# Kernel optimization log

Hardware: AMD Instinct MI355X
Metric: run time of the kernel (lower is better)

Reference implementation:

```python
import jax, jax.numpy as jnp
import numpy as np

N = 400_000
G = 160
C_IN, C_OUT = 64, 38
K = 27  # 3x3x3 kernel offsets


def _build_neighbor_map(rng):
    # sample N unique occupied voxel coordinates, sorted by ravelled key
    keys = np.sort(rng.choice(G ** 3, size=N, replace=False))
    coords = np.stack(np.unravel_index(keys, (G, G, G)), axis=1).astype(np.int64)  # [N,3]
    nbr = np.full((K, N), N, dtype=np.int32)  # N = padding index -> zero feature row
    k = 0
    for dx in (-1, 0, 1):
        for dy in (-1, 0, 1):
            for dz in (-1, 0, 1):
                nc = coords + np.array([dx, dy, dz])
                valid = np.all((nc >= 0) & (nc < G), axis=1)
                nkey = (nc[:, 0] * G + nc[:, 1]) * G + nc[:, 2]
                pos = np.searchsorted(keys, nkey)
                pos_c = np.clip(pos, 0, N - 1)
                found = valid & (keys[pos_c] == nkey)
                nbr[k] = np.where(found, pos_c, N).astype(np.int32)
                k += 1
    return nbr


def setup_inputs() -> dict:
    key = jax.random.key(0)
    k1, k2, k3 = jax.random.split(key, 3)
    rng = np.random.default_rng(0)
    neighbor_idx = jnp.asarray(_build_neighbor_map(rng))
    features = jax.random.normal(k1, (N, C_IN), dtype=jnp.float32)
    # kaiming_normal fan_out (relu): std = sqrt(2 / fan_out), fan_out = K * C_out
    std1 = (2.0 / (K * C_OUT)) ** 0.5
    std2 = (2.0 / (K * C_OUT)) ** 0.5
    W1 = jax.random.normal(k2, (K, C_IN, C_OUT), dtype=jnp.float32) * std1
    W2 = jax.random.normal(k3, (K, C_OUT, C_OUT), dtype=jnp.float32) * std2
    return {"features": features, "neighbor_idx": neighbor_idx, "W1": W1, "W2": W2}


def _sparse_conv(feat, W, neighbor_idx):
    # gather-GEMM-scatter: out[i] = sum_k W[k]^T feat[nbr[k,i]]
    fp = jnp.concatenate([feat, jnp.zeros((1, feat.shape[1]), feat.dtype)], axis=0)
    out = jnp.zeros((feat.shape[0], W.shape[2]), feat.dtype)
    for k in range(K):  # fixed structural loop over 27 kernel offsets
        out = out + fp[neighbor_idx[k]] @ W[k]
    return out


def reference(features, neighbor_idx, W1, W2):
    h = _sparse_conv(features, W1, neighbor_idx)
    h = jax.nn.gelu(h, approximate=False)  # torch nn.GELU default = exact
    return _sparse_conv(h, W2, neighbor_idx)
```

## Files before the change

kernel.cpp:

```cpp
#include <hip/hip_runtime.h>
#include <math.h>

#define NPTS 400000
#define K27  27
#define WSTRIDE 4096

typedef unsigned short u16;
typedef __bf16 bf16x8 __attribute__((ext_vector_type(8)));
typedef float  f32x4  __attribute__((ext_vector_type(4)));
typedef __attribute__((address_space(1))) void gvoid;
typedef __attribute__((address_space(3))) void lvoid;

__device__ __forceinline__ u16 f2bf(float f) {
    unsigned u = __float_as_uint(f);
    u += 0x7FFFu + ((u >> 16) & 1u);
    return (u16)(u >> 16);
}
__device__ __forceinline__ unsigned pack2(float lo, float hi) {
    return (unsigned)f2bf(lo) | ((unsigned)f2bf(hi) << 16);
}
__device__ __forceinline__ bf16x8 pack8(float4 x, float4 y) {
    union { uint4 u; bf16x8 v; } r;
    r.u.x = pack2(x.x, x.y); r.u.y = pack2(x.z, x.w);
    r.u.z = pack2(y.x, y.y); r.u.w = pack2(y.z, y.w);
    return r.v;
}
__device__ __forceinline__ bf16x8 zero8() {
    union { uint4 u; bf16x8 v; } r;
    r.u.x = 0; r.u.y = 0; r.u.z = 0; r.u.w = 0;
    return r.v;
}

__global__ void prep_w(const float* __restrict__ W1, const float* __restrict__ W2,
                       u16* __restrict__ W1t, u16* __restrict__ W2t,
                       u16* __restrict__ hpad, u16* __restrict__ fpad)
{
    int i = blockIdx.x * 256 + threadIdx.x;
    if (i < 64) {
        hpad[i] = 0;
        if (fpad) fpad[i] = 0;
    }
    const int TOT = K27 * 48 * 64;
    if (i >= TOT) return;
    int k  = i / (48 * 64);
    int r  = i % (48 * 64);
    int n  = r >> 6;
    int kc = r & 63;
    u16 w1 = 0, w2 = 0;
    if (n < 38) {
        w1 = f2bf(W1[(k * 64 + kc) * 38 + n]);
        if (kc < 38) w2 = f2bf(W2[(k * 38 + kc) * 38 + n]);
    }
    int os = r ^ ((n & 7) << 3);
    W1t[k * WSTRIDE + os] = w1;
    W2t[k * WSTRIDE + os] = w2;
}

__global__ void prep_feat(const float* __restrict__ F, u16* __restrict__ Fb)
{
    size_t i = (size_t)blockIdx.x * 256 + threadIdx.x;
    const size_t TOT = (size_t)NPTS * 64 / 8;
    if (i >= TOT) return;
    const float4* fp = (const float4*)(F + i * 8);
    float4 a = fp[0], b = fp[1];
    uint4 v;
    v.x = pack2(a.x, a.y); v.y = pack2(a.z, a.w);
    v.z = pack2(b.x, b.y); v.w = pack2(b.z, b.w);
    *(uint4*)(Fb + i * 8) = v;
}

template<int LAYER, bool BF16IN>
__global__ __launch_bounds__(256, 3)
void spconv(const void* __restrict__ in_, const int* __restrict__ nbr,
            const u16* __restrict__ Wt, void* __restrict__ out_)
{
    __shared__ __align__(16) u16 wbuf[2][WSTRIDE];

    const int t    = threadIdx.x;
    const int wave = t >> 6;
    const int lane = t & 63;
    const int quad = lane >> 4;
    const int l16  = lane & 15;

    int bid;
    {
        const int nwg = NPTS / 128, q = nwg / 8, r = nwg % 8;
        int x = blockIdx.x % 8, o = blockIdx.x / 8;
        bid = (x < r ? x * (q + 1) : r * (q + 1) + (x - r) * q) + o;
    }
    const int rbase = bid * 128 + wave * 32;
    const int swz   = (l16 & 7) << 3;

    f32x4 acc[2][3] = {};
    bf16x8 aP[2][2], aQ[2][2], aR[2][2];
    int jP[2], jQ[2], jR[2];

    #define GATHER_BF16(dst, ids)                                             \
        {                                                                     \
            const u16* F = (const u16*)in_;                                   \
            _Pragma("unroll")                                                 \
            for (int rt = 0; rt < 2; ++rt) {                                  \
                const u16* rowp = F + (size_t)(ids)[rt] * 64 + quad * 8;      \
                (dst)[rt][0] = *(const bf16x8*)(rowp);                        \
                (dst)[rt][1] = *(const bf16x8*)(rowp + 32);                   \
            }                                                                 \
        }
    #define GATHER_F32(dst, ids)                                              \
        {                                                                     \
            const float* F = (const float*)in_;                               \
            _Pragma("unroll")                                                 \
            for (int rt = 0; rt < 2; ++rt) {                                  \
                if ((ids)[rt] < NPTS) {                                       \
                    const float* rowp = F + (size_t)(ids)[rt] * 64 + quad * 8;\
                    float4 f0 = *(const float4*)(rowp);                       \
                    float4 f1 = *(const float4*)(rowp + 4);                   \
                    float4 f2 = *(const float4*)(rowp + 32);                  \
                    float4 f3 = *(const float4*)(rowp + 36);                  \
                    (dst)[rt][0] = pack8(f0, f1);                             \
                    (dst)[rt][1] = pack8(f2, f3);                             \
                } else {                                                      \
                    (dst)[rt][0] = zero8();                                   \
                    (dst)[rt][1] = zero8();                                   \
                }                                                             \
            }                                                                 \
        }
    #define GATHER(dst, ids) { if (BF16IN) GATHER_BF16(dst, ids) else GATHER_F32(dst, ids) }

    #define STAGE_W(KW, BSEL)                                                 \
        {                                                                     \
            const u16* g_ = Wt + (size_t)(KW) * WSTRIDE + t * 8;              \
            u16* l_ = &wbuf[(BSEL)][t * 8];                                   \
            __builtin_amdgcn_global_load_lds((gvoid*)(g_),                    \
                                             (lvoid*)(l_), 16, 0, 0);         \
            __builtin_amdgcn_global_load_lds((gvoid*)(g_ + 2048),             \
                                             (lvoid*)(l_ + 2048), 16, 0, 0);  \
        }

    {
        int i0[2], i1[2];
        #pragma unroll
        for (int rt = 0; rt < 2; ++rt) i0[rt] = nbr[rbase + rt * 16 + l16];
        GATHER(aP, i0);
        #pragma unroll
        for (int rt = 0; rt < 2; ++rt) i1[rt] = nbr[(size_t)NPTS + rbase + rt * 16 + l16];
        GATHER(aQ, i1);
        #pragma unroll
        for (int rt = 0; rt < 2; ++rt) jP[rt] = nbr[(size_t)2 * NPTS + rbase + rt * 16 + l16];
    }
    STAGE_W(0, 0);
    STAGE_W(1, 1);
    __builtin_amdgcn_sched_barrier(0);
    asm volatile("s_waitcnt vmcnt(2)");
    __builtin_amdgcn_s_barrier();
    __builtin_amdgcn_sched_barrier(0);

    #define ITER(KK, ACUR, AISS, JUSE, JLOAD)                                 \
      {                                                                       \
        const int k_ = (KK);                                                  \
        bf16x8 bfr[3][2];                                                     \
        {                                                                     \
            const u16* wb = &wbuf[k_ & 1][0];                                 \
            _Pragma("unroll")                                                 \
            for (int nt = 0; nt < 3; ++nt)                                    \
                _Pragma("unroll")                                             \
                for (int ks = 0; ks < 2; ++ks)                                \
                    bfr[nt][ks] = *(const bf16x8*)&wb[(nt * 16 + l16) * 64    \
                                        + ((ks * 32 + quad * 8) ^ swz)];      \
        }                                                                     \
        {                                                                     \
            int kf = k_ + 3; if (kf > K27 - 1) kf = K27 - 1;                  \
            const int* nr = nbr + (size_t)kf * NPTS + rbase;                  \
            _Pragma("unroll")                                                 \
            for (int rt = 0; rt < 2; ++rt) JLOAD[rt] = nr[rt * 16 + l16];     \
        }                                                                     \
        GATHER(AISS, JUSE);                                                   \
        __builtin_amdgcn_sched_barrier(0);                                    \
        __builtin_amdgcn_s_setprio(1);                                        \
        _Pragma("unroll")                                                     \
        for (int ks = 0; ks < 2; ++ks)                                        \
            _Pragma("unroll")                                                 \
            for (int rt = 0; rt < 2; ++rt)                                    \
                _Pragma("unroll")                                             \
                for (int nt = 0; nt < 3; ++nt)                                \
                    acc[rt][nt] = __builtin_amdgcn_mfma_f32_16x16x32_bf16(    \
                        ACUR[rt][ks], bfr[nt][ks], acc[rt][nt], 0, 0, 0);     \
        __builtin_amdgcn_s_setprio(0);                                        \
        __builtin_amdgcn_sched_barrier(0);                                    \
        if (BF16IN) { asm volatile("s_waitcnt vmcnt(6)"); }                   \
        else        { asm volatile("s_waitcnt vmcnt(10)"); }                  \
        __builtin_amdgcn_s_barrier();                                         \
        __builtin_amdgcn_sched_barrier(0);                                    \
        {                                                                     \
            int kw = k_ + 2; if (kw > K27 - 1) kw = K27 - 1;                  \
            STAGE_W(kw, k_ & 1);                                              \
        }                                                                     \
        __builtin_amdgcn_sched_barrier(0);                                    \
      }

    for (int k = 0; k < K27; k += 3) {
        ITER(k,     aP, aR, jP, jQ);
        ITER(k + 1, aQ, aP, jQ, jR);
        ITER(k + 2, aR, aQ, jR, jP);
    }

    if (LAYER == 1) {
        u16* h = (u16*)out_;
        #pragma unroll
        for (int rt = 0; rt < 2; ++rt) {
            #pragma unroll
            for (int r = 0; r < 4; ++r) {
                size_t ro = (size_t)(rbase + rt * 16 + quad * 4 + r) * 64;
                #pragma unroll
                for (int nt = 0; nt < 3; ++nt) {
                    float x = acc[rt][nt][r];
                    float g = 0.5f * x * (1.0f + erff(x * 0.70710678118654752f));
                    h[ro + nt * 16 + l16] = f2bf(g);
                }
                h[ro + 48 + l16] = 0;
            }
        }
    } else {
        float* out = (float*)out_;
        #pragma unroll
        for (int rt = 0; rt < 2; ++rt) {
            #pragma unroll
            for (int nt = 0; nt < 3; ++nt) {
                int col = nt * 16 + l16;
                if (col < 38) {
                    #pragma unroll
                    for (int r = 0; r < 4; ++r) {
                        int row = rbase + rt * 16 + quad * 4 + r;
                        out[(size_t)row * 38 + col] = acc[rt][nt][r];
                    }
                }
            }
        }
    }
    #undef ITER
    #undef STAGE_W
    #undef GATHER
    #undef GATHER_BF16
    #undef GATHER_F32
}

extern "C" void kernel_launch(void* const* d_in, const int* in_sizes, int n_in,
                              void* d_out, int out_size, void* d_ws, size_t ws_size,
                              hipStream_t stream)
{
    const float* feat = (const float*)d_in[0];
    const int*   nbr  = (const int*)  d_in[1];
    const float* W1   = (const float*)d_in[2];
    const float* W2   = (const float*)d_in[3];

    const size_t hbytes = (size_t)(NPTS + 1) * 64 * 2;
    const size_t wbytes = (size_t)K27 * WSTRIDE * 2;

    char* ws  = (char*)d_ws;
    u16* h    = (u16*)ws;
    u16* W1t  = (u16*)(ws + hbytes);
    u16* W2t  = (u16*)(ws + hbytes + wbytes);
    u16* Fb   = (u16*)(ws + hbytes + 2 * wbytes);
    const bool full = ws_size >= hbytes * 2 + 2 * wbytes;

    prep_w<<<(K27 * 48 * 64 + 255) / 256, 256, 0, stream>>>(
        W1, W2, W1t, W2t,
        h + (size_t)NPTS * 64,
        full ? Fb + (size_t)NPTS * 64 : (u16*)nullptr);

    const int nblk = NPTS / 128;
    if (full) {
        prep_feat<<<(int)(((size_t)NPTS * 64 / 8 + 255) / 256), 256, 0, stream>>>(feat, Fb);
        spconv<1, true ><<<nblk, 256, 0, stream>>>(Fb,   nbr, W1t, h);
    } else {
        spconv<1, false><<<nblk, 256, 0, stream>>>(feat, nbr, W1t, h);
    }
    spconv<2, true ><<<nblk, 256, 0, stream>>>(h, nbr, W2t, d_out);
}
```

Before: 415.1 us.

## Stage sparse-conv weights through registers instead of direct global-to-LDS loads

Replaces the asynchronous global_load_lds weight staging with per-thread register prefetch of the weights for offset k+3, written into the LDS double buffer after the barrier. The neighbor-index ring shrinks from three buffers to two, and the loop is unrolled by six with a peeled tail of three iterations. The aim is to take the LDS DMA path off the critical path and deepen the weight prefetch. In exchange it uses more VGPRs, adds explicit LDS store instructions, and relies on hand-tuned vmcnt values that must match the number of outstanding loads.

```diff
diff --git a/kernel.cpp b/kernel.cpp
--- a/kernel.cpp
+++ b/kernel.cpp
@@ -93,7 +93,8 @@
 
     f32x4 acc[2][3] = {};
     bf16x8 aP[2][2], aQ[2][2], aR[2][2];
-    int jP[2], jQ[2], jR[2];
+    int iP[2], iQ[2];
+    uint4 wA0, wA1, wB0, wB1;
 
     #define GATHER_BF16(dst, ids)                                             \
         {                                                                     \
@@ -126,7 +127,7 @@
         }
     #define GATHER(dst, ids) { if (BF16IN) GATHER_BF16(dst, ids) else GATHER_F32(dst, ids) }
 
-    #define STAGE_W(KW, BSEL)                                                 \
+    #define STAGE_W_LDS(KW, BSEL)                                             \
         {                                                                     \
             const u16* g_ = Wt + (size_t)(KW) * WSTRIDE + t * 8;              \
             u16* l_ = &wbuf[(BSEL)][t * 8];                                   \
@@ -145,18 +146,28 @@
         for (int rt = 0; rt < 2; ++rt) i1[rt] = nbr[(size_t)NPTS + rbase + rt * 16 + l16];
         GATHER(aQ, i1);
         #pragma unroll
-        for (int rt = 0; rt < 2; ++rt) jP[rt] = nbr[(size_t)2 * NPTS + rbase + rt * 16 + l16];
-    }
-    STAGE_W(0, 0);
-    STAGE_W(1, 1);
+        for (int rt = 0; rt < 2; ++rt) iP[rt] = nbr[(size_t)2 * NPTS + rbase + rt * 16 + l16];
+        const uint4* wp = (const uint4*)(Wt + (size_t)2 * WSTRIDE + t * 16);
+        wA0 = wp[0]; wA1 = wp[1];
+        STAGE_W_LDS(0, 0);
+        STAGE_W_LDS(1, 1);
+    }
     __builtin_amdgcn_sched_barrier(0);
-    asm volatile("s_waitcnt vmcnt(2)");
+    asm volatile("s_waitcnt vmcnt(0) lgkmcnt(0)" ::: "memory");
     __builtin_amdgcn_s_barrier();
     __builtin_amdgcn_sched_barrier(0);
 
-    #define ITER(KK, ACUR, AISS, JUSE, JLOAD)                                 \
+    #define ITER(KK, ACUR, AISS, ICUR, ILOAD, WWR0, WWR1, WLD0, WLD1)         \
       {                                                                       \
         const int k_ = (KK);                                                  \
+                   \
+        {                                                                     \
+            int kw = k_ + 3; if (kw > K27 - 1) kw = K27 - 1;                  \
+            const uint4* wp = (const uint4*)(Wt + (size_t)kw * WSTRIDE + t * 16);\
+            WLD0 = wp[0]; WLD1 = wp[1];                                       \
+        }                                                                     \
+        __builtin_amdgcn_sched_barrier(0);                                    \
+                              \
         bf16x8 bfr[3][2];                                                     \
         {                                                                     \
             const u16* wb = &wbuf[k_ & 1][0];                                 \
@@ -171,10 +182,11 @@
             int kf = k_ + 3; if (kf > K27 - 1) kf = K27 - 1;                  \
             const int* nr = nbr + (size_t)kf * NPTS + rbase;                  \
             _Pragma("unroll")                                                 \
-            for (int rt = 0; rt < 2; ++rt) JLOAD[rt] = nr[rt * 16 + l16];     \
-        }                                                                     \
-        GATHER(AISS, JUSE);                                                   \
-        __builtin_amdgcn_sched_barrier(0);                                    \
+            for (int rt = 0; rt < 2; ++rt) ILOAD[rt] = nr[rt * 16 + l16];     \
+        }                                                                     \
+        GATHER(AISS, ICUR);                                                   \
+        __builtin_amdgcn_sched_barrier(0);                                    \
+              \
         __builtin_amdgcn_s_setprio(1);                                        \
         _Pragma("unroll")                                                     \
         for (int ks = 0; ks < 2; ++ks)                                        \
@@ -186,22 +198,31 @@
                         ACUR[rt][ks], bfr[nt][ks], acc[rt][nt], 0, 0, 0);     \
         __builtin_amdgcn_s_setprio(0);                                        \
         __builtin_amdgcn_sched_barrier(0);                                    \
-        if (BF16IN) { asm volatile("s_waitcnt vmcnt(6)"); }                   \
-        else        { asm volatile("s_waitcnt vmcnt(10)"); }                  \
+                    \
         __builtin_amdgcn_s_barrier();                                         \
         __builtin_amdgcn_sched_barrier(0);                                    \
-        {                                                                     \
-            int kw = k_ + 2; if (kw > K27 - 1) kw = K27 - 1;                  \
-            STAGE_W(kw, k_ & 1);                                              \
+                   \
+        if (BF16IN) { asm volatile("s_waitcnt vmcnt(14)" ::: "memory"); }     \
+        else        { asm volatile("s_waitcnt vmcnt(22)" ::: "memory"); }     \
+        __builtin_amdgcn_sched_barrier(0);                                    \
+        {                                                                     \
+            uint4* wb = (uint4*)&wbuf[k_ & 1][t * 16];                        \
+            wb[0] = WWR0; wb[1] = WWR1;                                       \
         }                                                                     \
         __builtin_amdgcn_sched_barrier(0);                                    \
       }
 
-    for (int k = 0; k < K27; k += 3) {
-        ITER(k,     aP, aR, jP, jQ);
-        ITER(k + 1, aQ, aP, jQ, jR);
-        ITER(k + 2, aR, aQ, jR, jP);
-    }
+    for (int k = 0; k < 24; k += 6) {
+        ITER(k + 0, aP, aR, iP, iQ, wA0, wA1, wB0, wB1);
+        ITER(k + 1, aQ, aP, iQ, iP, wB0, wB1, wA0, wA1);
+        ITER(k + 2, aR, aQ, iP, iQ, wA0, wA1, wB0, wB1);
+        ITER(k + 3, aP, aR, iQ, iP, wB0, wB1, wA0, wA1);
+        ITER(k + 4, aQ, aP, iP, iQ, wA0, wA1, wB0, wB1);
+        ITER(k + 5, aR, aQ, iQ, iP, wB0, wB1, wA0, wA1);
+    }
+    ITER(24, aP, aR, iP, iQ, wA0, wA1, wB0, wB1);
+    ITER(25, aQ, aP, iQ, iP, wB0, wB1, wA0, wA1);
+    ITER(26, aR, aQ, iP, iQ, wA0, wA1, wB0, wB1);
 
     if (LAYER == 1) {
         u16* h = (u16*)out_;
@@ -237,7 +258,7 @@
         }
     }
     #undef ITER
-    #undef STAGE_W
+    #undef STAGE_W_LDS
     #undef GATHER
     #undef GATHER_BF16
     #undef GATHER_F32
```

Measured after the change: 417.4 us. Within noise of the previous version (+0.5%).
